# Kernel tuning notes

Measured on AMD Instinct MI355X. Metric: run time of the kernel, lower is better.

Reference implementation:

```python
import jax, jax.numpy as jnp
import numpy as np

B, N, K = 32, 64, 128          # batch, atoms per cell, channel width (128x0e + 128x1o)
R_MAX = 5.0
NUM_BESSEL = 8
P_CUT = 5                       # num_polynomial_cutoff
AVG_NEIGH = 16.0                # avg_num_neighbors
H_MLP = 512                     # hidden_dimensions_size, n_hidden_dimensions = 2
FEAT = 5 * K                    # ((num_interactions-1)*4 + 1) * 128 = 640


def silu(x):
    return x * jax.nn.sigmoid(x)


def _bessel_cutoff(r, mask):
    # Bessel radial basis * polynomial cutoff (MACE), masked on valid edges.
    n = jnp.arange(1, NUM_BESSEL + 1, dtype=r.dtype)
    rb = jnp.sqrt(2.0 / R_MAX) * jnp.sin(n * (jnp.pi / R_MAX) * r[..., None]) / r[..., None]
    u = r / R_MAX
    p = float(P_CUT)
    fc = 1.0 - 0.5 * (p + 1) * (p + 2) * u**P_CUT + p * (p + 2) * u**(P_CUT + 1) - 0.5 * p * (p + 1) * u**(P_CUT + 2)
    fc = fc * (u < 1.0)
    return rb * (fc * mask)[..., None]


def _sph(uvec):
    # Real spherical harmonics l=0,1,2 (component normalization), uvec: unit edge vectors.
    x, y, z = uvec[..., 0], uvec[..., 1], uvec[..., 2]
    s3, s5, s15 = 3.0**0.5, 5.0**0.5, 15.0**0.5
    Y0 = jnp.ones_like(x)[..., None]
    Y1 = jnp.stack([s3 * x, s3 * y, s3 * z], -1)
    Y2 = jnp.stack([s15 * x * y, s15 * y * z, 0.5 * s5 * (3 * z * z - 1.0),
                    s15 * x * z, 0.5 * s15 * (x * x - y * y)], -1)
    return Y0, Y1, Y2


def _radial_mlp(x, w0, b0, w1, b1, w2, b2, w3, b3):
    h = silu(x @ w0 + b0)
    h = silu(h @ w1 + b1)
    h = silu(h @ w2 + b2)
    return h @ w3 + b3


def setup_inputs() -> dict:
    key = jax.random.key(0)
    ks = jax.random.split(key, 32)
    f32 = jnp.float32

    def lin(k, fan_in, shape):
        return (jax.random.normal(k, shape, dtype=f32) / np.sqrt(fan_in)).astype(f32)

    inp = {
        "noisy_relative_positions": jax.random.uniform(ks[0], (B, N, 3), dtype=f32),
        "time": jax.random.uniform(ks[1], (B, 1), dtype=f32),
        "unit_cell": (11.0 * jnp.eye(3, dtype=f32) + 0.3 * jax.random.uniform(ks[2], (B, 3, 3), dtype=f32)),
        "w_embed": lin(ks[3], 1, (K,)),
        # interaction 1 radial MLP: 8 -> 64 -> 64 -> 64 -> 3*K (weights for l=0,1,2 paths)
        "r1_w0": lin(ks[4], NUM_BESSEL, (NUM_BESSEL, 64)), "r1_b0": jnp.zeros((64,), f32),
        "r1_w1": lin(ks[5], 64, (64, 64)), "r1_b1": jnp.zeros((64,), f32),
        "r1_w2": lin(ks[6], 64, (64, 64)), "r1_b2": jnp.zeros((64,), f32),
        "r1_w3": lin(ks[7], 64, (64, 3 * K)), "r1_b3": jnp.zeros((3 * K,), f32),
        "mix1_l0": lin(ks[8], K, (K, K)),
        "mix1_l1": lin(ks[9], K, (K, K)),
        "mix1_l2": lin(ks[10], K, (K, K)),
        # interaction 2 radial MLP: 8 -> 64 -> 64 -> 64 -> 2*K (paths 0e x 0e -> 0e, 1o x 1o -> 0e)
        "r2_w0": lin(ks[11], NUM_BESSEL, (NUM_BESSEL, 64)), "r2_b0": jnp.zeros((64,), f32),
        "r2_w1": lin(ks[12], 64, (64, 64)), "r2_b1": jnp.zeros((64,), f32),
        "r2_w2": lin(ks[13], 64, (64, 64)), "r2_b2": jnp.zeros((64,), f32),
        "r2_w3": lin(ks[14], 64, (64, 2 * K)), "r2_b3": jnp.zeros((2 * K,), f32),
        "mix2": lin(ks[15], K, (K, K)),
        # readout MLP: 641 -> 512 -> 512 -> 3
        "mlp_w0": lin(ks[16], FEAT + 1, (FEAT + 1, H_MLP)), "mlp_b0": jnp.zeros((H_MLP,), f32),
        "mlp_w1": lin(ks[17], H_MLP, (H_MLP, H_MLP)), "mlp_b1": jnp.zeros((H_MLP,), f32),
        "mlp_w2": lin(ks[18], H_MLP, (H_MLP, 3)), "mlp_b2": jnp.zeros((3,), f32),
    }
    return inp


def reference(noisy_relative_positions, time, unit_cell, w_embed,
              r1_w0, r1_b0, r1_w1, r1_b1, r1_w2, r1_b2, r1_w3, r1_b3,
              mix1_l0, mix1_l1, mix1_l2,
              r2_w0, r2_b0, r2_w1, r2_b1, r2_w2, r2_b2, r2_w3, r2_b3, mix2,
              mlp_w0, mlp_b0, mlp_w1, mlp_b1, mlp_w2, mlp_b2):
    frac = noisy_relative_positions                      # [B,N,3] fractional
    d = frac[:, :, None, :] - frac[:, None, :, :]        # [B,N,N,3]
    d = d - jnp.round(d)                                 # minimum-image PBC
    dc = jnp.einsum('bijc,bcd->bijd', d, unit_cell)      # cartesian displacements
    r = jnp.sqrt(jnp.maximum(jnp.sum(dc * dc, -1), 1e-12))
    mask = (r < R_MAX) & (~jnp.eye(N, dtype=bool))[None]
    r_safe = jnp.where(mask, r, 1.0)
    uvec = dc / r_safe[..., None] * mask[..., None]      # unit edge vectors (0 off-edge)

    rad = _bessel_cutoff(r_safe, mask)                   # [B,N,N,8]
    Y0, Y1, Y2 = _sph(uvec)                              # [B,N,N,1|3|5]

    h0 = jnp.broadcast_to(w_embed, (B, N, K))            # element embedding (single species)

    # ---- interaction 1: radial-weighted tensor product h_j (x) Y_l, scatter over j ----
    we = _radial_mlp(rad, r1_w0, r1_b0, r1_w1, r1_b1, r1_w2, r1_b2, r1_w3, r1_b3)
    we = we.reshape(B, N, N, 3, K) * mask[..., None, None]
    hj = h0[:, None, :, :]                               # sender features [B,1,N,K]
    msg0 = jnp.einsum('bijk,bijm->bimk', we[..., 0, :] * hj, Y0)[:, :, 0] / AVG_NEIGH  # [B,N,K]
    msg1 = jnp.einsum('bijk,bijm->bimk', we[..., 1, :] * hj, Y1) / AVG_NEIGH           # [B,N,3,K]
    msg2 = jnp.einsum('bijk,bijm->bimk', we[..., 2, :] * hj, Y2) / AVG_NEIGH           # [B,N,5,K]

    s1 = msg0 @ mix1_l0 + jnp.sum(msg2 * msg2, axis=2) @ mix1_l2   # scalars [B,N,K]
    v1 = jnp.einsum('bimk,kc->bimc', msg1, mix1_l1)                # vectors [B,N,3,K]
    h1 = silu(s1)

    # ---- interaction 2: scalar output from 0e x 0e and 1o x 1o -> 0e paths ----
    we2 = _radial_mlp(rad, r2_w0, r2_b0, r2_w1, r2_b1, r2_w2, r2_b2, r2_w3, r2_b3)
    we2 = we2.reshape(B, N, N, 2, K) * mask[..., None, None]
    msg_a = jnp.sum(we2[..., 0, :] * h1[:, None, :, :], axis=2)    # [B,N,K]
    inv = jnp.einsum('bijm,bjmk->bijk', Y1, v1)                    # Y1 . v1_j invariant
    msg_b = jnp.sum(we2[..., 1, :] * inv, axis=2)
    s2 = ((msg_a + msg_b) / AVG_NEIGH) @ mix2                      # [B,N,K]

    # node_feats: layer1 full irreps (128x0e + 128x1o -> 512) + layer2 scalars (128) = 640
    node_feats = jnp.concatenate([s1, v1.reshape(B, N, 3 * K), s2], axis=-1)

    t = jnp.broadcast_to(time[:, None, :], (B, N, 1))
    x = jnp.concatenate([node_feats, t], axis=-1)                  # [B,N,641]
    x = jax.nn.relu(x @ mlp_w0 + mlp_b0)
    x = jax.nn.relu(x @ mlp_w1 + mlp_b1)
    return x @ mlp_w2 + mlp_b2                                     # [B,N,3]
```

## Files before the change

kernel.cpp:

```cpp
#include <hip/hip_runtime.h>
#include <math.h>

#define B_ 32
#define N_ 64
#define K_ 128
#define NPAIR (B_*N_*N_)
#define PREP_TOTAL 733184

typedef __attribute__((ext_vector_type(8))) short short8;
typedef __attribute__((ext_vector_type(8))) __bf16 bf16x8;
typedef __attribute__((ext_vector_type(4))) float floatx4;

__device__ __forceinline__ float silu_f(float x) {
    return x / (1.0f + expf(-x));
}

__device__ __forceinline__ short f2bf(float x) {
    union { float f; unsigned u; } v; v.f = x;
    unsigned r = (v.u + 0x7FFFu + ((v.u >> 16) & 1u)) >> 16;
    return (short)r;
}
__device__ __forceinline__ float bf2f(short s) {
    union { unsigned u; float f; } v;
    v.u = ((unsigned)(unsigned short)s) << 16;
    return v.f;
}
__device__ __forceinline__ bf16x8 ld_frag(const short* p) {
    short8 r = *(const short8*)p;
    return __builtin_bit_cast(bf16x8, r);
}

__global__ __launch_bounds__(256) void prep_kernel(
    const float* __restrict__ r1w1, const float* __restrict__ r1w2,
    const float* __restrict__ r2w1, const float* __restrict__ r2w2,
    const float* __restrict__ r2w3, const float* __restrict__ mw0,
    const float* __restrict__ mw1,
    const float* __restrict__ r1w0, const float* __restrict__ r2w0,
    const float* __restrict__ r1w3,
    const float* __restrict__ l0, const float* __restrict__ l1,
    const float* __restrict__ l2,
    short* __restrict__ dst)
{
    int idx = blockIdx.x * 256 + threadIdx.x;
    if (idx >= PREP_TOTAL) return;
    short v;
    if (idx < 4096) {
        int h = idx >> 6, k = idx & 63; v = f2bf(r1w1[k*64 + h]);
    } else if (idx < 8192) {
        int i = idx - 4096; int h = i >> 6, k = i & 63; v = f2bf(r1w2[k*64 + h]);
    } else if (idx < 12288) {
        int i = idx - 8192; int h = i >> 6, k = i & 63; v = f2bf(r2w1[k*64 + h]);
    } else if (idx < 16384) {
        int i = idx - 12288; int h = i >> 6, k = i & 63; v = f2bf(r2w2[k*64 + h]);
    } else if (idx < 32768) {
        int i = idx - 16384; int col = i >> 6, h = i & 63; v = f2bf(r2w3[h*256 + col]);
    } else if (idx < 393216) {
        int i = idx - 32768; int n = i / 704, k = i - n*704;
        v = (k < 641) ? f2bf(mw0[(size_t)k*512 + n]) : (short)0;
    } else if (idx < 655360) {
        int i = idx - 393216; int n = i >> 9, k = i & 511;
        v = f2bf(mw1[(size_t)k*512 + n]);
    } else if (idx < 657408) {
        int i = idx - 655360; int h = i >> 5, k = i & 31;
        v = (k < 8) ? f2bf(r1w0[k*64 + h]) : (short)0;
    } else if (idx < 659456) {
        int i = idx - 657408; int h = i >> 5, k = i & 31;
        v = (k < 8) ? f2bf(r2w0[k*64 + h]) : (short)0;
    } else if (idx < 684032) {
        int i = idx - 659456; int col = i >> 6, h = i & 63;
        v = f2bf(r1w3[(size_t)h*384 + col]);
    } else {
        int i = idx - 684032; int n = i >> 7, k = i & 127;
        float src = (n < 128) ? l0[(size_t)k*128 + n]
                  : (n < 256) ? l1[(size_t)k*128 + (n-128)]
                              : l2[(size_t)k*128 + (n-256)];
        v = f2bf(src);
    }
    dst[idx] = v;
}

__global__ __launch_bounds__(256) void geom_kernel(
    const float* __restrict__ pos, const float* __restrict__ cell,
    float* __restrict__ rad, float* __restrict__ Y1, float* __restrict__ Y2,
    float* __restrict__ maskf)
{
    int p = blockIdx.x * 256 + threadIdx.x;
    if (p >= NPAIR) return;
    int b = p >> 12;
    int ij = p & 4095;
    int i = ij >> 6, j = ij & 63;
    const float* pi = pos + (size_t)(b*N_ + i)*3;
    const float* pj = pos + (size_t)(b*N_ + j)*3;
    float d0 = pi[0]-pj[0], d1 = pi[1]-pj[1], d2 = pi[2]-pj[2];
    d0 -= rintf(d0); d1 -= rintf(d1); d2 -= rintf(d2);
    const float* C = cell + b*9;
    float dc0 = d0*C[0] + d1*C[3] + d2*C[6];
    float dc1 = d0*C[1] + d1*C[4] + d2*C[7];
    float dc2 = d0*C[2] + d1*C[5] + d2*C[8];
    float r2 = fmaxf(dc0*dc0 + dc1*dc1 + dc2*dc2, 1e-12f);
    float r = sqrtf(r2);
    bool m = (r < 5.0f) && (i != j);
    float mf = m ? 1.0f : 0.0f;
    float rs = m ? r : 1.0f;
    float inv_rs = 1.0f / rs;
    float x = dc0*inv_rs*mf, y = dc1*inv_rs*mf, z = dc2*inv_rs*mf;
    float u = r * 0.2f;
    float u2 = u*u, u4 = u2*u2, u5 = u4*u;
    float fc = 1.0f - 21.0f*u5 + 35.0f*u5*u - 15.0f*u5*u2;
    fc = (u < 1.0f) ? fc : 0.0f;
    float pref = 0.6324555320336759f * inv_rs * (fc * mf);
    float w = 0.6283185307179586f * rs;
    float sw = sinf(w), cw = cosf(w);
    float twoc = 2.0f * cw;
    float sm = 0.0f, s = sw;
    #pragma unroll
    for (int n = 1; n <= 8; n++) {
        rad[(size_t)p*8 + (n-1)] = pref * s;
        float nx = twoc*s - sm;
        sm = s; s = nx;
    }
    const float s3  = 1.7320508075688772f;
    const float s5  = 2.23606797749979f;
    const float s15 = 3.872983346207417f;
    float* y1 = Y1 + (size_t)p*3;
    y1[0] = s3*x; y1[1] = s3*y; y1[2] = s3*z;
    float* y2 = Y2 + (size_t)p*5;
    y2[0] = s15*x*y;
    y2[1] = s15*y*z;
    y2[2] = 0.5f*s5*(3.0f*z*z - 1.0f);
    y2[3] = s15*x*z;
    y2[4] = 0.5f*s15*(x*x - y*y);
    maskf[p] = mf;
}

__device__ __forceinline__ void mfma_layer(
    const short* __restrict__ src, const short* __restrict__ WT,
    const float* __restrict__ bias, short* __restrict__ dst,
    int wv, int qd, int nn)
{
    floatx4 acc[4];
    #pragma unroll
    for (int tt = 0; tt < 4; tt++) acc[tt] = (floatx4){0.f, 0.f, 0.f, 0.f};
    #pragma unroll
    for (int ks = 0; ks < 64; ks += 32) {
        bf16x8 a = ld_frag(&src[(wv*16 + nn)*72 + ks + qd*8]);
        #pragma unroll
        for (int tt = 0; tt < 4; tt++) {
            bf16x8 b = ld_frag(&WT[(tt*16 + nn)*64 + ks + qd*8]);
            acc[tt] = __builtin_amdgcn_mfma_f32_16x16x32_bf16(a, b, acc[tt], 0, 0, 0);
        }
    }
    #pragma unroll
    for (int tt = 0; tt < 4; tt++) {
        int col = tt*16 + nn;
        float bv = bias[col];
        #pragma unroll
        for (int i = 0; i < 4; i++) {
            int row = wv*16 + qd*4 + i;
            dst[row*72 + col] = f2bf(silu_f(acc[tt][i] + bv));
        }
    }
}

__device__ __forceinline__ void mfma_layer_T(
    const short* __restrict__ src, const short* __restrict__ WT,
    const float* __restrict__ bias, short* __restrict__ dstT,
    int wv, int qd, int nn)
{
    floatx4 acc[4];
    #pragma unroll
    for (int tt = 0; tt < 4; tt++) acc[tt] = (floatx4){0.f, 0.f, 0.f, 0.f};
    #pragma unroll
    for (int ks = 0; ks < 64; ks += 32) {
        bf16x8 a = ld_frag(&src[(wv*16 + nn)*72 + ks + qd*8]);
        #pragma unroll
        for (int tt = 0; tt < 4; tt++) {
            bf16x8 b = ld_frag(&WT[(tt*16 + nn)*64 + ks + qd*8]);
            acc[tt] = __builtin_amdgcn_mfma_f32_16x16x32_bf16(a, b, acc[tt], 0, 0, 0);
        }
    }
    #pragma unroll
    for (int tt = 0; tt < 4; tt++) {
        int col = tt*16 + nn;
        float bv = bias[col];
        #pragma unroll
        for (int i = 0; i < 4; i++) {
            int row = wv*16 + qd*4 + i;
            dstT[col*72 + row] = f2bf(silu_f(acc[tt][i] + bv));
        }
    }
}

__device__ __forceinline__ void mfma_layer0(
    const short* __restrict__ rad_bf, const short* __restrict__ w0T,
    const float* __restrict__ b0, short* __restrict__ dst,
    int wv, int qd, int nn)
{
    floatx4 acc[4];
    #pragma unroll
    for (int tt = 0; tt < 4; tt++) acc[tt] = (floatx4){0.f, 0.f, 0.f, 0.f};
    bf16x8 a = ld_frag(&rad_bf[(wv*16 + nn)*32 + qd*8]);
    #pragma unroll
    for (int tt = 0; tt < 4; tt++) {
        bf16x8 b = ld_frag(&w0T[(tt*16 + nn)*32 + qd*8]);
        acc[tt] = __builtin_amdgcn_mfma_f32_16x16x32_bf16(a, b, acc[tt], 0, 0, 0);
    }
    #pragma unroll
    for (int tt = 0; tt < 4; tt++) {
        int col = tt*16 + nn;
        float bv = b0[col];
        #pragma unroll
        for (int i = 0; i < 4; i++) {
            int row = wv*16 + qd*4 + i;
            dst[row*72 + col] = f2bf(silu_f(acc[tt][i] + bv));
        }
    }
}

__global__ __launch_bounds__(256) void pass1_kernel(
    const float* __restrict__ rad, const float* __restrict__ Y1g,
    const float* __restrict__ Y2g, const float* __restrict__ maskg,
    const float* __restrict__ wemb,
    const short* __restrict__ w0T, const float* __restrict__ b0,
    const short* __restrict__ w1T, const float* __restrict__ b1,
    const short* __restrict__ w2T, const float* __restrict__ b2,
    const short* __restrict__ w3T, const float* __restrict__ b3,
    const short* __restrict__ lcatT, const float* __restrict__ timeg,
    float* __restrict__ h1g, float* __restrict__ v1g, short* __restrict__ featsb)
{
    __shared__ __align__(16) char smem[23040];
    short* actA   = (short*)smem;
    short* actB   = (short*)(smem + 9216);
    float* msg    = (float*)(smem + 9216);
    float* q_s    = (float*)(smem + 9216 + 4608);
    short* rad_bf = (short*)(smem + 18432);
    short* Ym_bf  = (short*)(smem + 18432);
    short* G_bf   = (short*)(smem + 18432 + 2304);
    short* A2     = (short*)smem;
    float* Psa    = (float*)(smem + 9216);
    float* Psb    = Psa + 128;

    int t = threadIdx.x;
    int wv = t >> 6, lane = t & 63, qd = lane >> 4, nn = lane & 15;
    int node = blockIdx.x;
    int b = node >> 6;
    size_t pbase = (size_t)node * 64;

    for (int idx = t; idx < 2048; idx += 256) {
        int j = idx >> 5, k = idx & 31;
        rad_bf[j*32 + k] = (k < 8) ? f2bf(rad[pbase*8 + j*8 + k]) : (short)0;
    }
    float vals[9];
    float sy9[9];
    if (t < 64) {
        int j = t;
        float mf = maskg[pbase + j];
        vals[0] = mf;
        #pragma unroll
        for (int m = 0; m < 3; m++) vals[1+m] = Y1g[(pbase+j)*3 + m] * mf;
        #pragma unroll
        for (int m = 0; m < 5; m++) vals[4+m] = Y2g[(pbase+j)*5 + m] * mf;
        #pragma unroll
        for (int m = 0; m < 9; m++) {
            float s = vals[m];
            #pragma unroll
            for (int off = 32; off > 0; off >>= 1) s += __shfl_xor(s, off);
            sy9[m] = s;
        }
    }
    __syncthreads();

    mfma_layer0(rad_bf, w0T, b0, actA, wv, qd, nn);
    __syncthreads();

    if (t < 64) {
        int j = t;
        #pragma unroll
        for (int m = 0; m < 9; m++) Ym_bf[m*72 + j] = f2bf(vals[m]);
        #pragma unroll
        for (int m = 9; m < 16; m++) Ym_bf[m*72 + j] = 0;
        #pragma unroll
        for (int m = 0; m < 9; m++)
            if (j == m) *(float*)(&Ym_bf[m*72 + 64]) = sy9[m];
    }
    mfma_layer(actA, w1T, b1, actB, wv, qd, nn);
    __syncthreads();

    mfma_layer_T(actB, w2T, b2, actA, wv, qd, nn);
    __syncthreads();

    {
        floatx4 acc = (floatx4){0.f, 0.f, 0.f, 0.f};
        #pragma unroll
        for (int ks = 0; ks < 64; ks += 32) {
            bf16x8 a = ld_frag(&Ym_bf[nn*72 + ks + qd*8]);
            bf16x8 bb = ld_frag(&actA[(wv*16 + nn)*72 + ks + qd*8]);
            acc = __builtin_amdgcn_mfma_f32_16x16x32_bf16(a, bb, acc, 0, 0, 0);
        }
        #pragma unroll
        for (int i = 0; i < 4; i++)
            G_bf[(qd*4 + i)*72 + wv*16 + nn] = f2bf(acc[i]);
    }
    __syncthreads();

    {
        floatx4 acc[6];
        #pragma unroll
        for (int tt = 0; tt < 6; tt++) acc[tt] = (floatx4){0.f, 0.f, 0.f, 0.f};
        #pragma unroll
        for (int ks = 0; ks < 64; ks += 32) {
            bf16x8 a = ld_frag(&G_bf[nn*72 + ks + qd*8]);
            #pragma unroll
            for (int tt = 0; tt < 6; tt++) {
                bf16x8 bb = ld_frag(&w3T[((wv*6 + tt)*16 + nn)*64 + ks + qd*8]);
                acc[tt] = __builtin_amdgcn_mfma_f32_16x16x32_bf16(a, bb, acc[tt], 0, 0, 0);
            }
        }
        #pragma unroll
        for (int tt = 0; tt < 6; tt++) {
            int col = (wv*6 + tt)*16 + nn;
            #pragma unroll
            for (int i = 0; i < 4; i++) {
                int m = qd*4 + i;
                if (m < 9) {
                    int c = (m == 0) ? 0 : ((m < 4) ? 1 : 2);
                    int k = col - c*128;
                    if (k >= 0 && k < 128) {
                        float sym = *(const float*)(&Ym_bf[m*72 + 64]);
                        msg[m*128 + k] = (acc[tt][i] + sym*b3[col]) * wemb[k] * 0.0625f;
                    }
                }
            }
        }
    }
    __syncthreads();

    if (t < 128) {
        int k = t;
        float acc = 0.f;
        #pragma unroll
        for (int m = 4; m < 9; m++) { float v = msg[m*128 + k]; acc += v*v; }
        q_s[k] = acc;
    }
    __syncthreads();

    for (int idx = t; idx < 2048; idx += 256) {
        int r = idx >> 7, k = idx & 127;
        float v = (r == 0) ? msg[k]
                : (r == 1) ? q_s[k]
                : (r < 5)  ? msg[(r-1)*128 + k] : 0.f;
        A2[r*136 + k] = f2bf(v);
    }
    __syncthreads();

    {
        bf16x8 pa[4];
        #pragma unroll
        for (int ksI = 0; ksI < 4; ksI++)
            pa[ksI] = ld_frag(&A2[nn*136 + ksI*32 + qd*8]);
        floatx4 acc[6];
        #pragma unroll
        for (int tt = 0; tt < 6; tt++) acc[tt] = (floatx4){0.f, 0.f, 0.f, 0.f};
        #pragma unroll
        for (int tt = 0; tt < 6; tt++) {
            int tn = wv*6 + tt;
            #pragma unroll
            for (int ksI = 0; ksI < 4; ksI++) {
                bf16x8 bf = ld_frag(&lcatT[((size_t)(tn*16 + nn))*128 + ksI*32 + qd*8]);
                acc[tt] = __builtin_amdgcn_mfma_f32_16x16x32_bf16(pa[ksI], bf, acc[tt], 0, 0, 0);
            }
        }
        #pragma unroll
        for (int tt = 0; tt < 6; tt++) {
            int n = (wv*6 + tt)*16 + nn;
            #pragma unroll
            for (int i = 0; i < 4; i++) {
                int r = qd*4 + i;
                float val = acc[tt][i];
                if (r == 0 && n < 128) Psa[n] = val;
                else if (r == 1 && n >= 256) Psb[n - 256] = val;
                else if (r >= 2 && r < 5 && n >= 128 && n < 256) {
                    int m = r - 2, cc = n - 128;
                    v1g[(size_t)node*384 + m*128 + cc] = val;
                    featsb[(size_t)node*704 + 128 + m*128 + cc] = f2bf(val);
                }
            }
        }
    }
    __syncthreads();

    if (t < 128) {
        float s1 = Psa[t] + Psb[t];
        featsb[(size_t)node*704 + t] = f2bf(s1);
        h1g[(size_t)node*128 + t] = silu_f(s1);
    } else if (t == 128) {
        featsb[(size_t)node*704 + 640] = f2bf(timeg[b]);
    } else if (t > 128 && t < 192) {
        featsb[(size_t)node*704 + 640 + (t - 128)] = 0;
    }
}

__global__ __launch_bounds__(256) void pass2_kernel(
    const float* __restrict__ rad, const float* __restrict__ Y1g,
    const float* __restrict__ maskg,
    const short* __restrict__ w0T, const float* __restrict__ b0,
    const short* __restrict__ w1T, const float* __restrict__ b1,
    const short* __restrict__ w2T, const float* __restrict__ b2,
    const short* __restrict__ w3T, const float* __restrict__ b3,
    const float* __restrict__ mix2,
    const float* __restrict__ h1g, const float* __restrict__ v1g,
    short* __restrict__ featsb)
{
    __shared__ __align__(16) char smem[22528];
    short* actA   = (short*)smem;
    short* actB   = (short*)(smem + 9216);
    short* rad_bf = (short*)(smem + 18432);
    float* aux    = (float*)(smem + 18432);
    float* mask_s = aux;
    float* Y1s    = aux + 64;
    float* msgab  = aux + 320;

    int t = threadIdx.x;
    int wv = t >> 6, lane = t & 63, qd = lane >> 4, nn = lane & 15;
    int node = blockIdx.x;
    int b = node >> 6;
    size_t pbase = (size_t)node * 64;

    for (int idx = t; idx < 2048; idx += 256) {
        int j = idx >> 5, k = idx & 31;
        rad_bf[j*32 + k] = (k < 8) ? f2bf(rad[pbase*8 + j*8 + k]) : (short)0;
    }
    float pmf = 0.f, py0 = 0.f, py1 = 0.f, py2 = 0.f;
    if (t < 64) {
        pmf = maskg[pbase + t];
        py0 = Y1g[(pbase+t)*3 + 0];
        py1 = Y1g[(pbase+t)*3 + 1];
        py2 = Y1g[(pbase+t)*3 + 2];
    }
    __syncthreads();

    mfma_layer0(rad_bf, w0T, b0, actA, wv, qd, nn);
    __syncthreads();

    if (t < 64) {
        mask_s[t] = pmf;
        Y1s[t*4 + 0] = py0; Y1s[t*4 + 1] = py1; Y1s[t*4 + 2] = py2;
    }
    if (t < 128) msgab[t] = 0.f;
    mfma_layer(actA, w1T, b1, actB, wv, qd, nn);
    __syncthreads();

    mfma_layer(actB, w2T, b2, actA, wv, qd, nn);
    __syncthreads();

    for (int g = 0; g < 4; g++) {
        floatx4 acc[4];
        #pragma unroll
        for (int tt = 0; tt < 4; tt++) acc[tt] = (floatx4){0.f, 0.f, 0.f, 0.f};
        #pragma unroll
        for (int ks = 0; ks < 64; ks += 32) {
            bf16x8 a = ld_frag(&actA[(wv*16 + nn)*72 + ks + qd*8]);
            #pragma unroll
            for (int tt = 0; tt < 4; tt++) {
                int col0 = g*64 + tt*16;
                bf16x8 bb = ld_frag(&w3T[(col0 + nn)*64 + ks + qd*8]);
                acc[tt] = __builtin_amdgcn_mfma_f32_16x16x32_bf16(a, bb, acc[tt], 0, 0, 0);
            }
        }
        #pragma unroll
        for (int tt = 0; tt < 4; tt++) {
            int col = g*64 + tt*16 + nn;
            float bias = b3[col];
            int k = col & 127;
            float p = 0.f;
            if (col < 128) {
                #pragma unroll
                for (int i = 0; i < 4; i++) {
                    int j = wv*16 + qd*4 + i;
                    float we = (acc[tt][i] + bias) * mask_s[j];
                    p += we * h1g[((size_t)b*64 + j)*128 + k];
                }
            } else {
                #pragma unroll
                for (int i = 0; i < 4; i++) {
                    int j = wv*16 + qd*4 + i;
                    float we = (acc[tt][i] + bias) * mask_s[j];
                    const float* vb = &v1g[((size_t)b*64 + j)*384 + k];
                    float inv = Y1s[j*4+0]*vb[0] + Y1s[j*4+1]*vb[128] + Y1s[j*4+2]*vb[256];
                    p += we * inv;
                }
            }
            p += __shfl_xor(p, 16);
            p += __shfl_xor(p, 32);
            if (qd == 0) atomicAdd(&msgab[k], p);
        }
    }
    __syncthreads();

    if (t < 128) {
        int c = t;
        float acc = 0.f;
        for (int k = 0; k < 128; k++) acc += msgab[k] * mix2[k*128 + c];
        featsb[(size_t)node*704 + 512 + c] = f2bf(acc * 0.0625f);
    }
}

__global__ __launch_bounds__(256) void gemm_mfma_kernel(
    const short* __restrict__ A, int lda,
    const short* __restrict__ BT, int ldb, int K,
    const float* __restrict__ bias, short* __restrict__ Cout, int ldo)
{
    __shared__ short As[64*72];
    __shared__ short Bs[64*72];
    int t = threadIdx.x;
    int wv = t >> 6, lane = t & 63, qd = lane >> 4, nn = lane & 15;
    int m0 = blockIdx.x * 64, n0 = blockIdx.y * 64;
    floatx4 acc[4];
    #pragma unroll
    for (int tt = 0; tt < 4; tt++) acc[tt] = (floatx4){0.f, 0.f, 0.f, 0.f};

    for (int kc = 0; kc < K; kc += 64) {
        for (int s = t; s < 512; s += 256) {
            int j = s >> 3, kk = (s & 7) * 8;
            *(uint4*)&As[j*72 + kk] = *(const uint4*)&A[(size_t)(m0 + j)*lda + kc + kk];
            *(uint4*)&Bs[j*72 + kk] = *(const uint4*)&BT[(size_t)(n0 + j)*ldb + kc + kk];
        }
        __syncthreads();
        #pragma unroll
        for (int ks = 0; ks < 64; ks += 32) {
            bf16x8 a = ld_frag(&As[(wv*16 + nn)*72 + ks + qd*8]);
            #pragma unroll
            for (int tt = 0; tt < 4; tt++) {
                bf16x8 bb = ld_frag(&Bs[(tt*16 + nn)*72 + ks + qd*8]);
                acc[tt] = __builtin_amdgcn_mfma_f32_16x16x32_bf16(a, bb, acc[tt], 0, 0, 0);
            }
        }
        __syncthreads();
    }
    #pragma unroll
    for (int tt = 0; tt < 4; tt++) {
        int n = n0 + tt*16 + nn;
        float bv = bias[n];
        #pragma unroll
        for (int i = 0; i < 4; i++) {
            int m = m0 + wv*16 + qd*4 + i;
            Cout[(size_t)m*ldo + n] = f2bf(fmaxf(acc[tt][i] + bv, 0.f));
        }
    }
}

__global__ __launch_bounds__(64) void final3_kernel(
    const short* __restrict__ H, const float* __restrict__ w2,
    const float* __restrict__ b2, float* __restrict__ out)
{
    int node = blockIdx.x, lane = threadIdx.x;
    float a0 = 0.f, a1 = 0.f, a2 = 0.f;
    #pragma unroll
    for (int r = 0; r < 8; r++) {
        int k = r*64 + lane;
        float h = bf2f(H[(size_t)node*512 + k]);
        a0 += h * w2[k*3 + 0];
        a1 += h * w2[k*3 + 1];
        a2 += h * w2[k*3 + 2];
    }
    #pragma unroll
    for (int off = 32; off > 0; off >>= 1) {
        a0 += __shfl_down(a0, off);
        a1 += __shfl_down(a1, off);
        a2 += __shfl_down(a2, off);
    }
    if (lane == 0) {
        out[(size_t)node*3 + 0] = a0 + b2[0];
        out[(size_t)node*3 + 1] = a1 + b2[1];
        out[(size_t)node*3 + 2] = a2 + b2[2];
    }
}

extern "C" void kernel_launch(void* const* d_in, const int* in_sizes, int n_in,
                              void* d_out, int out_size, void* d_ws, size_t ws_size,
                              hipStream_t stream) {
    const float* pos   = (const float*)d_in[0];
    const float* timeg = (const float*)d_in[1];
    const float* cell  = (const float*)d_in[2];
    const float* wemb  = (const float*)d_in[3];
    const float* r1w0  = (const float*)d_in[4];
    const float* r1b0  = (const float*)d_in[5];
    const float* r1w1  = (const float*)d_in[6];
    const float* r1b1  = (const float*)d_in[7];
    const float* r1w2  = (const float*)d_in[8];
    const float* r1b2  = (const float*)d_in[9];
    const float* r1w3  = (const float*)d_in[10];
    const float* r1b3  = (const float*)d_in[11];
    const float* l0    = (const float*)d_in[12];
    const float* l1    = (const float*)d_in[13];
    const float* l2    = (const float*)d_in[14];
    const float* r2w0  = (const float*)d_in[15];
    const float* r2b0  = (const float*)d_in[16];
    const float* r2w1  = (const float*)d_in[17];
    const float* r2b1  = (const float*)d_in[18];
    const float* r2w2  = (const float*)d_in[19];
    const float* r2b2  = (const float*)d_in[20];
    const float* r2w3  = (const float*)d_in[21];
    const float* r2b3  = (const float*)d_in[22];
    const float* mix2  = (const float*)d_in[23];
    const float* mw0   = (const float*)d_in[24];
    const float* mb0   = (const float*)d_in[25];
    const float* mw1   = (const float*)d_in[26];
    const float* mb1   = (const float*)d_in[27];
    const float* mw2   = (const float*)d_in[28];
    const float* mb2   = (const float*)d_in[29];

    float* ws    = (float*)d_ws;
    float* rad   = ws;
    float* Y1    = rad   + (size_t)NPAIR*8;
    float* Y2    = Y1    + (size_t)NPAIR*3;
    float* maskf = Y2    + (size_t)NPAIR*5;
    float* h1    = maskf + (size_t)NPAIR;
    float* v1    = h1    + (size_t)B_*N_*K_;
    short* featsb = (short*)(v1 + (size_t)B_*N_*3*K_);
    short* prep  = featsb + (size_t)2048*704;
    short* w1T_1 = prep;
    short* w2T_1 = prep + 4096;
    short* w1T_2 = prep + 8192;
    short* w2T_2 = prep + 12288;
    short* w3T_2 = prep + 16384;
    short* wT0   = prep + 32768;
    short* wT1   = prep + 393216;
    short* w0T_1 = prep + 655360;
    short* w0T_2 = prep + 657408;
    short* w3T_1 = prep + 659456;
    short* lcatT = prep + 684032;
    short* h0bb = (short*)rad;
    short* h1bb = (short*)Y2;

    prep_kernel<<<(PREP_TOTAL + 255)/256, 256, 0, stream>>>(
        r1w1, r1w2, r2w1, r2w2, r2w3, mw0, mw1,
        r1w0, r2w0, r1w3, l0, l1, l2, prep);
    geom_kernel<<<NPAIR/256, 256, 0, stream>>>(pos, cell, rad, Y1, Y2, maskf);
    pass1_kernel<<<B_*N_, 256, 0, stream>>>(rad, Y1, Y2, maskf, wemb,
        w0T_1, r1b0, w1T_1, r1b1, w2T_1, r1b2, w3T_1, r1b3, lcatT, timeg,
        h1, v1, featsb);
    pass2_kernel<<<B_*N_, 256, 0, stream>>>(rad, Y1, maskf,
        w0T_2, r2b0, w1T_2, r2b1, w2T_2, r2b2, w3T_2, r2b3, mix2, h1, v1, featsb);
    dim3 g0(32, 8);
    gemm_mfma_kernel<<<g0, 256, 0, stream>>>(featsb, 704, wT0, 704, 704, mb0, h0bb, 512);
    gemm_mfma_kernel<<<g0, 256, 0, stream>>>(h0bb, 512, wT1, 512, 512, mb1, h1bb, 512);
    final3_kernel<<<B_*N_, 64, 0, stream>>>(h1bb, mw2, mb2, (float*)d_out);
}
```

Before: 290.2 us.

## Fuse geometry and both radial MLP front layers into pass1 kernel

Removes the separate geometry kernel and computes edge distances, Bessel basis and spherical harmonics inline in the pass1 kernel. Pass1 now also runs the first three layers of the interaction-2 radial MLP and writes the bf16 hidden activations to global memory. Pass2 is reduced to the final layer plus the message contraction, reading a compact float4 mask/Y1 buffer instead of the rad/Y1/Y2/mask arrays. This cuts a launch and the duplicated radial MLP setup, at the cost of larger shared memory in pass1 (lower occupancy) and a new 16 MB intermediate buffer round trip.

```diff
diff --git a/kernel.cpp b/kernel.cpp
--- a/kernel.cpp
+++ b/kernel.cpp
@@ -79,60 +79,6 @@
     dst[idx] = v;
 }
 
-__global__ __launch_bounds__(256) void geom_kernel(
-    const float* __restrict__ pos, const float* __restrict__ cell,
-    float* __restrict__ rad, float* __restrict__ Y1, float* __restrict__ Y2,
-    float* __restrict__ maskf)
-{
-    int p = blockIdx.x * 256 + threadIdx.x;
-    if (p >= NPAIR) return;
-    int b = p >> 12;
-    int ij = p & 4095;
-    int i = ij >> 6, j = ij & 63;
-    const float* pi = pos + (size_t)(b*N_ + i)*3;
-    const float* pj = pos + (size_t)(b*N_ + j)*3;
-    float d0 = pi[0]-pj[0], d1 = pi[1]-pj[1], d2 = pi[2]-pj[2];
-    d0 -= rintf(d0); d1 -= rintf(d1); d2 -= rintf(d2);
-    const float* C = cell + b*9;
-    float dc0 = d0*C[0] + d1*C[3] + d2*C[6];
-    float dc1 = d0*C[1] + d1*C[4] + d2*C[7];
-    float dc2 = d0*C[2] + d1*C[5] + d2*C[8];
-    float r2 = fmaxf(dc0*dc0 + dc1*dc1 + dc2*dc2, 1e-12f);
-    float r = sqrtf(r2);
-    bool m = (r < 5.0f) && (i != j);
-    float mf = m ? 1.0f : 0.0f;
-    float rs = m ? r : 1.0f;
-    float inv_rs = 1.0f / rs;
-    float x = dc0*inv_rs*mf, y = dc1*inv_rs*mf, z = dc2*inv_rs*mf;
-    float u = r * 0.2f;
-    float u2 = u*u, u4 = u2*u2, u5 = u4*u;
-    float fc = 1.0f - 21.0f*u5 + 35.0f*u5*u - 15.0f*u5*u2;
-    fc = (u < 1.0f) ? fc : 0.0f;
-    float pref = 0.6324555320336759f * inv_rs * (fc * mf);
-    float w = 0.6283185307179586f * rs;
-    float sw = sinf(w), cw = cosf(w);
-    float twoc = 2.0f * cw;
-    float sm = 0.0f, s = sw;
-    #pragma unroll
-    for (int n = 1; n <= 8; n++) {
-        rad[(size_t)p*8 + (n-1)] = pref * s;
-        float nx = twoc*s - sm;
-        sm = s; s = nx;
-    }
-    const float s3  = 1.7320508075688772f;
-    const float s5  = 2.23606797749979f;
-    const float s15 = 3.872983346207417f;
-    float* y1 = Y1 + (size_t)p*3;
-    y1[0] = s3*x; y1[1] = s3*y; y1[2] = s3*z;
-    float* y2 = Y2 + (size_t)p*5;
-    y2[0] = s15*x*y;
-    y2[1] = s15*y*z;
-    y2[2] = 0.5f*s5*(3.0f*z*z - 1.0f);
-    y2[3] = s15*x*z;
-    y2[4] = 0.5f*s15*(x*x - y*y);
-    maskf[p] = mf;
-}
-
 __device__ __forceinline__ void mfma_layer(
     const short* __restrict__ src, const short* __restrict__ WT,
     const float* __restrict__ bias, short* __restrict__ dst,
@@ -191,6 +137,35 @@
     }
 }
 
+__device__ __forceinline__ void mfma_layer_gout(
+    const short* __restrict__ src, const short* __restrict__ WT,
+    const float* __restrict__ bias, short* __restrict__ gdst,
+    int wv, int qd, int nn)
+{
+    floatx4 acc[4];
+    #pragma unroll
+    for (int tt = 0; tt < 4; tt++) acc[tt] = (floatx4){0.f, 0.f, 0.f, 0.f};
+    #pragma unroll
+    for (int ks = 0; ks < 64; ks += 32) {
+        bf16x8 a = ld_frag(&src[(wv*16 + nn)*72 + ks + qd*8]);
+        #pragma unroll
+        for (int tt = 0; tt < 4; tt++) {
+            bf16x8 b = ld_frag(&WT[(tt*16 + nn)*64 + ks + qd*8]);
+            acc[tt] = __builtin_amdgcn_mfma_f32_16x16x32_bf16(a, b, acc[tt], 0, 0, 0);
+        }
+    }
+    #pragma unroll
+    for (int tt = 0; tt < 4; tt++) {
+        int col = tt*16 + nn;
+        float bv = bias[col];
+        #pragma unroll
+        for (int i = 0; i < 4; i++) {
+            int row = wv*16 + qd*4 + i;
+            gdst[row*64 + col] = f2bf(silu_f(acc[tt][i] + bv));
+        }
+    }
+}
+
 __device__ __forceinline__ void mfma_layer0(
     const short* __restrict__ rad_bf, const short* __restrict__ w0T,
     const float* __restrict__ b0, short* __restrict__ dst,
@@ -217,25 +192,30 @@
     }
 }
 
-__global__ __launch_bounds__(256) void pass1_kernel(
-    const float* __restrict__ rad, const float* __restrict__ Y1g,
-    const float* __restrict__ Y2g, const float* __restrict__ maskg,
+__global__ __launch_bounds__(256) void pass1x_kernel(
+    const float* __restrict__ pos, const float* __restrict__ cell,
     const float* __restrict__ wemb,
-    const short* __restrict__ w0T, const float* __restrict__ b0,
-    const short* __restrict__ w1T, const float* __restrict__ b1,
-    const short* __restrict__ w2T, const float* __restrict__ b2,
-    const short* __restrict__ w3T, const float* __restrict__ b3,
+    const short* __restrict__ w0T1, const float* __restrict__ b01,
+    const short* __restrict__ w1T1, const float* __restrict__ b11,
+    const short* __restrict__ w2T1, const float* __restrict__ b21,
+    const short* __restrict__ w3T1, const float* __restrict__ b31,
+    const short* __restrict__ w0T2, const float* __restrict__ b02,
+    const short* __restrict__ w1T2, const float* __restrict__ b12,
+    const short* __restrict__ w2T2, const float* __restrict__ b22,
     const short* __restrict__ lcatT, const float* __restrict__ timeg,
+    float* __restrict__ geo4, short* __restrict__ hc2,
     float* __restrict__ h1g, float* __restrict__ v1g, short* __restrict__ featsb)
 {
-    __shared__ __align__(16) char smem[23040];
+    __shared__ __align__(16) char smem[41472];
     short* actA   = (short*)smem;
     short* actB   = (short*)(smem + 9216);
+    short* actC   = (short*)(smem + 18432);
+    short* actD   = (short*)(smem + 27648);
     float* msg    = (float*)(smem + 9216);
     float* q_s    = (float*)(smem + 9216 + 4608);
-    short* rad_bf = (short*)(smem + 18432);
-    short* Ym_bf  = (short*)(smem + 18432);
-    short* G_bf   = (short*)(smem + 18432 + 2304);
+    short* rad_bf = (short*)(smem + 36864);
+    short* Ym_bf  = (short*)(smem + 36864);
+    short* G_bf   = (short*)(smem + 36864 + 2304);
     short* A2     = (short*)smem;
     float* Psa    = (float*)(smem + 9216);
     float* Psb    = Psa + 128;
@@ -244,49 +224,86 @@
     int wv = t >> 6, lane = t & 63, qd = lane >> 4, nn = lane & 15;
     int node = blockIdx.x;
     int b = node >> 6;
+    int irow = node & 63;
     size_t pbase = (size_t)node * 64;
 
-    for (int idx = t; idx < 2048; idx += 256) {
-        int j = idx >> 5, k = idx & 31;
-        rad_bf[j*32 + k] = (k < 8) ? f2bf(rad[pbase*8 + j*8 + k]) : (short)0;
-    }
     float vals[9];
     float sy9[9];
     if (t < 64) {
         int j = t;
-        float mf = maskg[pbase + j];
+        const float* pi = pos + (size_t)(b*N_ + irow)*3;
+        const float* pj = pos + (size_t)(b*N_ + j)*3;
+        float d0 = pi[0]-pj[0], d1 = pi[1]-pj[1], d2 = pi[2]-pj[2];
+        d0 -= rintf(d0); d1 -= rintf(d1); d2 -= rintf(d2);
+        const float* C = cell + b*9;
+        float dc0 = d0*C[0] + d1*C[3] + d2*C[6];
+        float dc1 = d0*C[1] + d1*C[4] + d2*C[7];
+        float dc2 = d0*C[2] + d1*C[5] + d2*C[8];
+        float r2 = fmaxf(dc0*dc0 + dc1*dc1 + dc2*dc2, 1e-12f);
+        float r = sqrtf(r2);
+        bool m = (r < 5.0f) && (irow != j);
+        float mf = m ? 1.0f : 0.0f;
+        float rs = m ? r : 1.0f;
+        float inv_rs = 1.0f / rs;
+        float x = dc0*inv_rs*mf, y = dc1*inv_rs*mf, z = dc2*inv_rs*mf;
+        float u = r * 0.2f;
+        float u2 = u*u, u4 = u2*u2, u5 = u4*u;
+        float fc = 1.0f - 21.0f*u5 + 35.0f*u5*u - 15.0f*u5*u2;
+        fc = (u < 1.0f) ? fc : 0.0f;
+        float pref = 0.6324555320336759f * inv_rs * (fc * mf);
+        float w = 0.6283185307179586f * rs;
+        float sw = sinf(w), cw = cosf(w);
+        float twoc = 2.0f * cw;
+        float sm = 0.0f, s = sw;
+        #pragma unroll
+        for (int n = 0; n < 8; n++) {
+            rad_bf[j*32 + n] = f2bf(pref * s);
+            float nx = twoc*s - sm;
+            sm = s; s = nx;
+        }
+        #pragma unroll
+        for (int k = 8; k < 32; k++) rad_bf[j*32 + k] = 0;
+        const float s3  = 1.7320508075688772f;
+        const float s5  = 2.23606797749979f;
+        const float s15 = 3.872983346207417f;
         vals[0] = mf;
-        #pragma unroll
-        for (int m = 0; m < 3; m++) vals[1+m] = Y1g[(pbase+j)*3 + m] * mf;
-        #pragma unroll
-        for (int m = 0; m < 5; m++) vals[4+m] = Y2g[(pbase+j)*5 + m] * mf;
-        #pragma unroll
-        for (int m = 0; m < 9; m++) {
-            float s = vals[m];
+        vals[1] = s3*x; vals[2] = s3*y; vals[3] = s3*z;
+        vals[4] = s15*x*y;
+        vals[5] = s15*y*z;
+        vals[6] = 0.5f*s5*(3.0f*z*z - 1.0f);
+        vals[7] = s15*x*z;
+        vals[8] = 0.5f*s15*(x*x - y*y);
+        *(float4*)&geo4[(pbase + j)*4] = make_float4(mf, vals[1], vals[2], vals[3]);
+        #pragma unroll
+        for (int m9 = 0; m9 < 9; m9++) {
+            float sv = vals[m9];
             #pragma unroll
-            for (int off = 32; off > 0; off >>= 1) s += __shfl_xor(s, off);
-            sy9[m] = s;
-        }
-    }
-    __syncthreads();
-
-    mfma_layer0(rad_bf, w0T, b0, actA, wv, qd, nn);
+            for (int off = 32; off > 0; off >>= 1) sv += __shfl_xor(sv, off);
+            sy9[m9] = sv;
+        }
+    }
+    __syncthreads();
+
+    mfma_layer0(rad_bf, w0T1, b01, actA, wv, qd, nn);
+    mfma_layer0(rad_bf, w0T2, b02, actC, wv, qd, nn);
     __syncthreads();
 
     if (t < 64) {
         int j = t;
         #pragma unroll
-        for (int m = 0; m < 9; m++) Ym_bf[m*72 + j] = f2bf(vals[m]);
-        #pragma unroll
-        for (int m = 9; m < 16; m++) Ym_bf[m*72 + j] = 0;
-        #pragma unroll
-        for (int m = 0; m < 9; m++)
-            if (j == m) *(float*)(&Ym_bf[m*72 + 64]) = sy9[m];
-    }
-    mfma_layer(actA, w1T, b1, actB, wv, qd, nn);
-    __syncthreads();
-
-    mfma_layer_T(actB, w2T, b2, actA, wv, qd, nn);
+        for (int m9 = 0; m9 < 9; m9++) Ym_bf[m9*72 + j] = f2bf(vals[m9]);
+        #pragma unroll
+        for (int m9 = 9; m9 < 16; m9++) Ym_bf[m9*72 + j] = 0;
+        #pragma unroll
+        for (int m9 = 0; m9 < 9; m9++)
+            if (j == m9) *(float*)(&Ym_bf[m9*72 + 64]) = sy9[m9];
+    }
+    mfma_layer(actA, w1T1, b11, actB, wv, qd, nn);
+    mfma_layer(actC, w1T2, b12, actD, wv, qd, nn);
+    __syncthreads();
+
+    mfma_layer_T(actB, w2T1, b21, actA, wv, qd, nn);
+    mfma_layer_gout(actD, w2T2, b22, hc2 + (size_t)node*4096, wv, qd, nn);
     __syncthreads();
 
     {
@@ -312,7 +329,7 @@
             bf16x8 a = ld_frag(&G_bf[nn*72 + ks + qd*8]);
             #pragma unroll
             for (int tt = 0; tt < 6; tt++) {
-                bf16x8 bb = ld_frag(&w3T[((wv*6 + tt)*16 + nn)*64 + ks + qd*8]);
+                bf16x8 bb = ld_frag(&w3T1[((wv*6 + tt)*16 + nn)*64 + ks + qd*8]);
                 acc[tt] = __builtin_amdgcn_mfma_f32_16x16x32_bf16(a, bb, acc[tt], 0, 0, 0);
             }
         }
@@ -321,13 +338,13 @@
             int col = (wv*6 + tt)*16 + nn;
             #pragma unroll
             for (int i = 0; i < 4; i++) {
-                int m = qd*4 + i;
-                if (m < 9) {
-                    int c = (m == 0) ? 0 : ((m < 4) ? 1 : 2);
+                int m9 = qd*4 + i;
+                if (m9 < 9) {
+                    int c = (m9 == 0) ? 0 : ((m9 < 4) ? 1 : 2);
                     int k = col - c*128;
                     if (k >= 0 && k < 128) {
-                        float sym = *(const float*)(&Ym_bf[m*72 + 64]);
-                        msg[m*128 + k] = (acc[tt][i] + sym*b3[col]) * wemb[k] * 0.0625f;
+                        float sym = *(const float*)(&Ym_bf[m9*72 + 64]);
+                        msg[m9*128 + k] = (acc[tt][i] + sym*b31[col]) * wemb[k] * 0.0625f;
                     }
                 }
             }
@@ -339,7 +356,7 @@
         int k = t;
         float acc = 0.f;
         #pragma unroll
-        for (int m = 4; m < 9; m++) { float v = msg[m*128 + k]; acc += v*v; }
+        for (int m9 = 4; m9 < 9; m9++) { float v = msg[m9*128 + k]; acc += v*v; }
         q_s[k] = acc;
     }
     __syncthreads();
@@ -380,9 +397,9 @@
                 if (r == 0 && n < 128) Psa[n] = val;
                 else if (r == 1 && n >= 256) Psb[n - 256] = val;
                 else if (r >= 2 && r < 5 && n >= 128 && n < 256) {
-                    int m = r - 2, cc = n - 128;
-                    v1g[(size_t)node*384 + m*128 + cc] = val;
-                    featsb[(size_t)node*704 + 128 + m*128 + cc] = f2bf(val);
+                    int m9 = r - 2, cc = n - 128;
+                    v1g[(size_t)node*384 + m9*128 + cc] = val;
+                    featsb[(size_t)node*704 + 128 + m9*128 + cc] = f2bf(val);
                 }
             }
         }
@@ -400,76 +417,49 @@
     }
 }
 
-__global__ __launch_bounds__(256) void pass2_kernel(
-    const float* __restrict__ rad, const float* __restrict__ Y1g,
-    const float* __restrict__ maskg,
-    const short* __restrict__ w0T, const float* __restrict__ b0,
-    const short* __restrict__ w1T, const float* __restrict__ b1,
-    const short* __restrict__ w2T, const float* __restrict__ b2,
+__global__ __launch_bounds__(256) void pass2b_kernel(
+    const float* __restrict__ geo4,
+    const short* __restrict__ hc2,
     const short* __restrict__ w3T, const float* __restrict__ b3,
     const float* __restrict__ mix2,
     const float* __restrict__ h1g, const float* __restrict__ v1g,
     short* __restrict__ featsb)
 {
-    __shared__ __align__(16) char smem[22528];
-    short* actA   = (short*)smem;
-    short* actB   = (short*)(smem + 9216);
-    short* rad_bf = (short*)(smem + 18432);
-    float* aux    = (float*)(smem + 18432);
-    float* mask_s = aux;
-    float* Y1s    = aux + 64;
-    float* msgab  = aux + 320;
-
+    __shared__ float mask_s[64];
+    __shared__ float Y1s[64*4];
+    __shared__ float msgab[128];
     int t = threadIdx.x;
     int wv = t >> 6, lane = t & 63, qd = lane >> 4, nn = lane & 15;
     int node = blockIdx.x;
     int b = node >> 6;
     size_t pbase = (size_t)node * 64;
 
-    for (int idx = t; idx < 2048; idx += 256) {
-        int j = idx >> 5, k = idx & 31;
-        rad_bf[j*32 + k] = (k < 8) ? f2bf(rad[pbase*8 + j*8 + k]) : (short)0;
-    }
-    float pmf = 0.f, py0 = 0.f, py1 = 0.f, py2 = 0.f;
     if (t < 64) {
-        pmf = maskg[pbase + t];
-        py0 = Y1g[(pbase+t)*3 + 0];
-        py1 = Y1g[(pbase+t)*3 + 1];
-        py2 = Y1g[(pbase+t)*3 + 2];
-    }
-    __syncthreads();
-
-    mfma_layer0(rad_bf, w0T, b0, actA, wv, qd, nn);
-    __syncthreads();
-
-    if (t < 64) {
-        mask_s[t] = pmf;
-        Y1s[t*4 + 0] = py0; Y1s[t*4 + 1] = py1; Y1s[t*4 + 2] = py2;
-    }
-    if (t < 128) msgab[t] = 0.f;
-    mfma_layer(actA, w1T, b1, actB, wv, qd, nn);
-    __syncthreads();
-
-    mfma_layer(actB, w2T, b2, actA, wv, qd, nn);
-    __syncthreads();
-
+        float4 g = *(const float4*)&geo4[(pbase + t)*4];
+        mask_s[t] = g.x;
+        Y1s[t*4 + 0] = g.y; Y1s[t*4 + 1] = g.z; Y1s[t*4 + 2] = g.w;
+    }
+    if (t >= 64 && t < 192) msgab[t - 64] = 0.f;
+    __syncthreads();
+
+    const short* hcb = hc2 + (size_t)node*4096;
+    bf16x8 a0 = ld_frag(&hcb[(wv*16 + nn)*64 + qd*8]);
+    bf16x8 a1 = ld_frag(&hcb[(wv*16 + nn)*64 + 32 + qd*8]);
     for (int g = 0; g < 4; g++) {
         floatx4 acc[4];
         #pragma unroll
         for (int tt = 0; tt < 4; tt++) acc[tt] = (floatx4){0.f, 0.f, 0.f, 0.f};
         #pragma unroll
-        for (int ks = 0; ks < 64; ks += 32) {
-            bf16x8 a = ld_frag(&actA[(wv*16 + nn)*72 + ks + qd*8]);
-            #pragma unroll
-            for (int tt = 0; tt < 4; tt++) {
-                int col0 = g*64 + tt*16;
-                bf16x8 bb = ld_frag(&w3T[(col0 + nn)*64 + ks + qd*8]);
-                acc[tt] = __builtin_amdgcn_mfma_f32_16x16x32_bf16(a, bb, acc[tt], 0, 0, 0);
-            }
-        }
-        #pragma unroll
         for (int tt = 0; tt < 4; tt++) {
-            int col = g*64 + tt*16 + nn;
+            int ct = g*4 + tt;
+            bf16x8 b0f = ld_frag(&w3T[(ct*16 + nn)*64 + qd*8]);
+            bf16x8 b1f = ld_frag(&w3T[(ct*16 + nn)*64 + 32 + qd*8]);
+            acc[tt] = __builtin_amdgcn_mfma_f32_16x16x32_bf16(a0, b0f, acc[tt], 0, 0, 0);
+            acc[tt] = __builtin_amdgcn_mfma_f32_16x16x32_bf16(a1, b1f, acc[tt], 0, 0, 0);
+        }
+        #pragma unroll
+        for (int tt = 0; tt < 4; tt++) {
+            int col = (g*4 + tt)*16 + nn;
             float bias = b3[col];
             int k = col & 127;
             float p = 0.f;
@@ -611,12 +601,9 @@
     const float* mb2   = (const float*)d_in[29];
 
     float* ws    = (float*)d_ws;
-    float* rad   = ws;
-    float* Y1    = rad   + (size_t)NPAIR*8;
-    float* Y2    = Y1    + (size_t)NPAIR*3;
-    float* maskf = Y2    + (size_t)NPAIR*5;
-    float* h1    = maskf + (size_t)NPAIR;
-    float* v1    = h1    + (size_t)B_*N_*K_;
+    float* geo4  = ws;
+    float* h1    = geo4 + (size_t)NPAIR*4;
+    float* v1    = h1   + (size_t)B_*N_*K_;
     short* featsb = (short*)(v1 + (size_t)B_*N_*3*K_);
     short* prep  = featsb + (size_t)2048*704;
     short* w1T_1 = prep;
@@ -630,18 +617,19 @@
     short* w0T_2 = prep + 657408;
     short* w3T_1 = prep + 659456;
     short* lcatT = prep + 684032;
-    short* h0bb = (short*)rad;
-    short* h1bb = (short*)Y2;
+    short* hc2   = prep + PREP_TOTAL;
+    short* h0bb  = hc2 + (size_t)2048*4096;
+    short* h1bb  = h0bb + (size_t)2048*512;
 
     prep_kernel<<<(PREP_TOTAL + 255)/256, 256, 0, stream>>>(
         r1w1, r1w2, r2w1, r2w2, r2w3, mw0, mw1,
         r1w0, r2w0, r1w3, l0, l1, l2, prep);
-    geom_kernel<<<NPAIR/256, 256, 0, stream>>>(pos, cell, rad, Y1, Y2, maskf);
-    pass1_kernel<<<B_*N_, 256, 0, stream>>>(rad, Y1, Y2, maskf, wemb,
-        w0T_1, r1b0, w1T_1, r1b1, w2T_1, r1b2, w3T_1, r1b3, lcatT, timeg,
-        h1, v1, featsb);
-    pass2_kernel<<<B_*N_, 256, 0, stream>>>(rad, Y1, maskf,
-        w0T_2, r2b0, w1T_2, r2b1, w2T_2, r2b2, w3T_2, r2b3, mix2, h1, v1, featsb);
+    pass1x_kernel<<<B_*N_, 256, 0, stream>>>(pos, cell, wemb,
+        w0T_1, r1b0, w1T_1, r1b1, w2T_1, r1b2, w3T_1, r1b3,
+        w0T_2, r2b0, w1T_2, r2b1, w2T_2, r2b2,
+        lcatT, timeg, geo4, hc2, h1, v1, featsb);
+    pass2b_kernel<<<B_*N_, 256, 0, stream>>>(geo4, hc2,
+        w3T_2, r2b3, mix2, h1, v1, featsb);
     dim3 g0(32, 8);
     gemm_mfma_kernel<<<g0, 256, 0, stream>>>(featsb, 704, wT0, 704, 704, mb0, h0bb, 512);
     gemm_mfma_kernel<<<g0, 256, 0, stream>>>(h0bb, 512, wT1, 512, 512, mb1, h1bb, 512);
```

New measurement: 288.5 us. Within noise of the previous version (-0.6%).
